# Kernel optimization log

Measured on AMD Instinct MI355X. Metric: run time of the kernel, lower is better.

Reference implementation:

```python
import jax, jax.numpy as jnp
import numpy as np

B, S, D = 16, 1024, 1024

def _xavier_uniform(key, shape, fan_in, fan_out):
    a = float(np.sqrt(6.0 / (fan_in + fan_out)))
    return jax.random.uniform(key, shape, jnp.float32, -a, a)

def setup_inputs() -> dict:
    key = jax.random.key(0)
    ks = jax.random.split(key, 8)
    query = jax.random.normal(ks[0], (B, S, D), jnp.float32)
    key_t = jax.random.normal(ks[1], (B, S, D), jnp.float32)
    value = jax.random.normal(ks[2], (B, S, D), jnp.float32)
    # learned additive attention bias [1, S, S], xavier_uniform init
    attn_bias = _xavier_uniform(ks[3], (1, S, S), S, S)
    # Linear weights (torch nn.Linear default: kaiming-uniform-ish; any init ok for baseline)
    Wq = _xavier_uniform(ks[4], (D, D), D, D)
    bq = jnp.zeros((D,), jnp.float32)
    Wk = _xavier_uniform(ks[5], (D, D), D, D)
    bk = jnp.zeros((D,), jnp.float32)
    return {"query": query, "key": key_t, "value": value,
            "attn_bias": attn_bias, "Wq": Wq, "bq": bq, "Wk": Wk, "bk": bk}

def reference(query, key, value, attn_bias, Wq, bq, Wk, bk):
    # q = query @ Wq^T + bq  (torch Linear convention)
    q = jnp.einsum('bsd,ed->bse', query, Wq) + bq            # [B,S,D]
    k = jnp.einsum('bsd,ed->bse', key, Wk) + bk              # [B,S,D]
    energy = jnp.einsum('bsd,btd->bst', q, k) + attn_bias    # [B,S,S] (bias broadcasts over B)
    attention = jax.nn.softmax(energy, axis=-1)
    out = jnp.einsum('bst,btd->bsd', attention, value)       # value is NOT projected (matches source)
    return (out, attention)
```

## Files before the change

kernel.cpp:

```cpp
#include <hip/hip_runtime.h>


#define AS1 __attribute__((address_space(1)))
#define AS3 __attribute__((address_space(3)))
#define VMCNT(n) asm volatile("s_waitcnt vmcnt(" #n ")" ::: "memory")

typedef __bf16 bf16;
typedef __bf16 bf16x4 __attribute__((ext_vector_type(4)));
typedef __bf16 bf16x8 __attribute__((ext_vector_type(8)));
typedef float  f32x4  __attribute__((ext_vector_type(4)));

constexpr int BATCH = 16;
constexpr int S = 1024;
constexpr int D = 1024;
constexpr long NBSD = (long)BATCH * S * D;

constexpr int GBM = 256, GBN = 256, GBK = 32;
constexpr int NTK = 1024 / GBK;
constexpr int ARR = GBM * GBK;

__device__ __forceinline__ void stage16(const bf16* src, const bf16* dst) {
  __builtin_amdgcn_global_load_lds((const AS1 void*)src, (AS3 void*)dst, 16, 0, 0);
}

__global__ __launch_bounds__(256) void split_convert(
    const float* __restrict__ in, bf16* __restrict__ hi, bf16* __restrict__ lo, int n4) {
  int i = blockIdx.x * blockDim.x + threadIdx.x;
  int stride = gridDim.x * blockDim.x;
  for (; i < n4; i += stride) {
    f32x4 x = ((const f32x4*)in)[i];
    bf16x4 h, l;
#pragma unroll
    for (int j = 0; j < 4; ++j) {
      float v = x[j];
      bf16 hh = (bf16)v;
      h[j] = hh;
      l[j] = (bf16)(v - (float)hh);
    }
    ((bf16x4*)hi)[i] = h;
    ((bf16x4*)lo)[i] = l;
  }
}

__global__ __launch_bounds__(256) void transpose_convert(
    const float* __restrict__ v, bf16* __restrict__ vT) {
  __shared__ float tile[32][33];
  const int b = blockIdx.z;
  const int t0 = blockIdx.y * 32, d0 = blockIdx.x * 32;
  const int tx = threadIdx.x & 31, ty = threadIdx.x >> 5;
  const float* src = v + (long)b * S * D;
#pragma unroll
  for (int i = 0; i < 4; ++i)
    tile[ty + i * 8][tx] = src[(long)(t0 + ty + i * 8) * D + d0 + tx];
  __syncthreads();
  bf16* dst = vT + (long)b * D * S;
#pragma unroll
  for (int i = 0; i < 4; ++i)
    dst[(long)(d0 + ty + i * 8) * S + t0 + tx] = (bf16)tile[tx][ty + i * 8];
}

template <int EPI>
__global__ __launch_bounds__(512, 2) void gemm8_split(
    const bf16* __restrict__ Ah_g, const bf16* __restrict__ Al_g, long a_bs,
    const bf16* __restrict__ Bh_g, const bf16* __restrict__ Bl_g, long b_bs,
    const float* __restrict__ bias,
    bf16* __restrict__ Ch, bf16* __restrict__ Cl,
    float* __restrict__ Cf, long c_bs) {
  __shared__ bf16 lds[2 * 4 * ARR];

  const int tid = threadIdx.x;
  const int lane = tid & 63, wid = tid >> 6;
  const int wr = wid >> 2, wc = wid & 3;
  const int fr = lane & 15, fq = lane >> 4;
  const int fsw = (fr >> 1) & 3;

  const int w = blockIdx.x;
  const int swz = (w & 7) * 32 + (w >> 3);
  int z, by, bx;
  if constexpr (EPI == 0) { z = 0; by = swz >> 2; bx = swz & 3; }
  else { z = swz >> 4; by = (swz >> 2) & 3; bx = swz & 3; }
  const long brow = (long)by * GBM, bcol = (long)bx * GBN;

  const bf16* A_h = Ah_g + (long)z * a_bs;
  const bf16* A_l = Al_g + (long)z * a_bs;
  const bf16* B_h = Bh_g + (long)z * b_bs;
  const bf16* B_l = Bl_g + (long)z * b_bs;

  const int srow = tid >> 2;
  const int csw = ((tid & 3) ^ ((srow >> 1) & 3)) * 8;
  const long asrc = (brow + srow) * 1024 + csw;
  const long bsrc = (bcol + srow) * 1024 + csw;
  const int dstoff = wid * 512;

  const int aoffb = (wr * 128 + fr) * 32 + (fq ^ fsw) * 8;
  const int boffb = (wc * 64 + fr) * 32 + (fq ^ fsw) * 8;

  f32x4 acc[8][4] = {};

#define STG(slot, arr, base, koff, rr) \
  stage16((base) + (koff) + (long)(rr) * 131072, \
          lds + ((slot) * 4 + (arr)) * ARR + (rr) * 4096 + dstoff)

  STG(0, 0, A_h + asrc, 0, 0); STG(0, 0, A_h + asrc, 0, 1);
  STG(0, 2, B_h + bsrc, 0, 0); STG(0, 2, B_h + bsrc, 0, 1);
  STG(0, 3, B_l + bsrc, 0, 0); STG(0, 3, B_l + bsrc, 0, 1);
  STG(0, 1, A_l + asrc, 0, 0); STG(0, 1, A_l + asrc, 0, 1);
  VMCNT(4);
  __builtin_amdgcn_s_barrier();

  for (int t = 0; t < NTK; ++t) {
    const int cur = t & 1, nxt = cur ^ 1;
    const long kn = (long)(t + 1) * GBK;
    const bf16* lA_h = lds + (cur * 4 + 0) * ARR;
    const bf16* lA_l = lds + (cur * 4 + 1) * ARR;
    const bf16* lB_h = lds + (cur * 4 + 2) * ARR;
    const bf16* lB_l = lds + (cur * 4 + 3) * ARR;

    bf16x8 ah[8], bh[4];
#pragma unroll
    for (int m = 0; m < 8; ++m) ah[m] = *(const bf16x8*)&lA_h[aoffb + m * 512];
#pragma unroll
    for (int n = 0; n < 4; ++n) bh[n] = *(const bf16x8*)&lB_h[boffb + n * 512];
    if (t + 1 < NTK) {
      STG(nxt, 0, A_h + asrc, kn, 0); STG(nxt, 0, A_h + asrc, kn, 1);
      STG(nxt, 2, B_h + bsrc, kn, 0); STG(nxt, 2, B_h + bsrc, kn, 1);
      VMCNT(6);
    } else { VMCNT(2); }
    __builtin_amdgcn_sched_barrier(0);
    __builtin_amdgcn_s_barrier();
    __builtin_amdgcn_s_setprio(1);
#pragma unroll
    for (int n = 0; n < 4; ++n)
#pragma unroll
      for (int m = 0; m < 8; ++m)
        acc[m][n] = __builtin_amdgcn_mfma_f32_16x16x32_bf16(ah[m], bh[n], acc[m][n], 0, 0, 0);
    __builtin_amdgcn_s_setprio(0);
    __builtin_amdgcn_sched_barrier(0);
    __builtin_amdgcn_s_barrier();

    bf16x8 bl[4];
#pragma unroll
    for (int n = 0; n < 4; ++n) bl[n] = *(const bf16x8*)&lB_l[boffb + n * 512];
    if (t + 1 < NTK) {
      STG(nxt, 3, B_l + bsrc, kn, 0); STG(nxt, 3, B_l + bsrc, kn, 1);
      VMCNT(6);
    } else { VMCNT(0); }
    __builtin_amdgcn_sched_barrier(0);
    __builtin_amdgcn_s_barrier();
    __builtin_amdgcn_s_setprio(1);
#pragma unroll
    for (int n = 0; n < 4; ++n)
#pragma unroll
      for (int m = 0; m < 8; ++m)
        acc[m][n] = __builtin_amdgcn_mfma_f32_16x16x32_bf16(ah[m], bl[n], acc[m][n], 0, 0, 0);
    __builtin_amdgcn_s_setprio(0);
    __builtin_amdgcn_sched_barrier(0);
    __builtin_amdgcn_s_barrier();

    bf16x8 al[8];
#pragma unroll
    for (int m = 0; m < 8; ++m) al[m] = *(const bf16x8*)&lA_l[aoffb + m * 512];
    if (t + 1 < NTK) {
      STG(nxt, 1, A_l + asrc, kn, 0); STG(nxt, 1, A_l + asrc, kn, 1);
      VMCNT(4);
    }
    __builtin_amdgcn_sched_barrier(0);
    __builtin_amdgcn_s_barrier();
    __builtin_amdgcn_s_setprio(1);
#pragma unroll
    for (int n = 0; n < 4; ++n)
#pragma unroll
      for (int m = 0; m < 8; ++m)
        acc[m][n] = __builtin_amdgcn_mfma_f32_16x16x32_bf16(al[m], bh[n], acc[m][n], 0, 0, 0);
    __builtin_amdgcn_s_setprio(0);
    __builtin_amdgcn_sched_barrier(0);
    __builtin_amdgcn_s_barrier();
  }
#undef STG

  if constexpr (EPI == 0) {
#pragma unroll
    for (int n = 0; n < 4; ++n) {
      const long col = bcol + wc * 64 + n * 16 + fr;
      const float bv = bias[col];
#pragma unroll
      for (int m = 0; m < 8; ++m) {
        const long row0 = brow + wr * 128 + m * 16 + fq * 4;
#pragma unroll
        for (int j = 0; j < 4; ++j) {
          const float c = acc[m][n][j] + bv;
          const bf16 h = (bf16)c;
          const bf16 l = (bf16)(c - (float)h);
          const long idx = (row0 + j) * 1024 + col;
          Ch[idx] = h;
          Cl[idx] = l;
        }
      }
    }
  } else {
    float* Cz = Cf + (long)z * c_bs;
#pragma unroll
    for (int n = 0; n < 4; ++n) {
      const long col = bcol + wc * 64 + n * 16 + fr;
#pragma unroll
      for (int m = 0; m < 8; ++m) {
        const long row0 = brow + wr * 128 + m * 16 + fq * 4;
#pragma unroll
        for (int j = 0; j < 4; ++j) {
          const long row = row0 + j;
          Cz[row * 1024 + col] = acc[m][n][j] + bias[row * 1024 + col];
        }
      }
    }
  }
}

__global__ __launch_bounds__(512, 2) void gemm8_plain(
    const bf16* __restrict__ A_g, long a_bs,
    const bf16* __restrict__ B_g, long b_bs,
    float* __restrict__ C, long c_bs) {
  __shared__ bf16 lds[3 * 2 * ARR];

  const int tid = threadIdx.x;
  const int lane = tid & 63, wid = tid >> 6;
  const int wr = wid >> 2, wc = wid & 3;
  const int fr = lane & 15, fq = lane >> 4;
  const int fsw = (fr >> 1) & 3;

  const int w = blockIdx.x;
  const int swz = (w & 7) * 32 + (w >> 3);
  const int z = swz >> 4, by = (swz >> 2) & 3, bx = swz & 3;
  const long brow = (long)by * GBM, bcol = (long)bx * GBN;

  const bf16* A = A_g + (long)z * a_bs;
  const bf16* B = B_g + (long)z * b_bs;

  const int srow = tid >> 2;
  const int csw = ((tid & 3) ^ ((srow >> 1) & 3)) * 8;
  const long asrc = (brow + srow) * 1024 + csw;
  const long bsrc = (bcol + srow) * 1024 + csw;
  const int dstoff = wid * 512;

  const int aoffb = (wr * 128 + fr) * 32 + (fq ^ fsw) * 8;
  const int boffb = (wc * 64 + fr) * 32 + (fq ^ fsw) * 8;

  f32x4 acc[8][4] = {};

#define STG2(slot, arr, base, koff, rr) \
  stage16((base) + (koff) + (long)(rr) * 131072, \
          lds + ((slot) * 2 + (arr)) * ARR + (rr) * 4096 + dstoff)

  STG2(0, 0, A + asrc, 0, 0);  STG2(0, 0, A + asrc, 0, 1);
  STG2(0, 1, B + bsrc, 0, 0);  STG2(0, 1, B + bsrc, 0, 1);
  STG2(1, 0, A + asrc, 32, 0); STG2(1, 0, A + asrc, 32, 1);
  STG2(1, 1, B + bsrc, 32, 0); STG2(1, 1, B + bsrc, 32, 1);
  VMCNT(4);
  __builtin_amdgcn_s_barrier();

  int cur = 0, st = 2;
  for (int t = 0; t < NTK; ++t) {
    const bf16* lA = lds + (cur * 2 + 0) * ARR;
    const bf16* lB = lds + (cur * 2 + 1) * ARR;
    bf16x8 ah[8], bh[4];
#pragma unroll
    for (int m = 0; m < 8; ++m) ah[m] = *(const bf16x8*)&lA[aoffb + m * 512];
#pragma unroll
    for (int n = 0; n < 4; ++n) bh[n] = *(const bf16x8*)&lB[boffb + n * 512];
    if (t + 2 < NTK) {
      const long kn = (long)(t + 2) * GBK;
      STG2(st, 0, A + asrc, kn, 0); STG2(st, 0, A + asrc, kn, 1);
      STG2(st, 1, B + bsrc, kn, 0); STG2(st, 1, B + bsrc, kn, 1);
      VMCNT(4);
    } else { VMCNT(0); }
    __builtin_amdgcn_sched_barrier(0);
    __builtin_amdgcn_s_barrier();
    __builtin_amdgcn_s_setprio(1);
#pragma unroll
    for (int n = 0; n < 4; ++n)
#pragma unroll
      for (int m = 0; m < 8; ++m)
        acc[m][n] = __builtin_amdgcn_mfma_f32_16x16x32_bf16(ah[m], bh[n], acc[m][n], 0, 0, 0);
    __builtin_amdgcn_s_setprio(0);
    __builtin_amdgcn_sched_barrier(0);
    __builtin_amdgcn_s_barrier();
    cur = (cur == 2) ? 0 : cur + 1;
    st  = (st == 2)  ? 0 : st + 1;
  }
#undef STG2

  float* Cz = C + (long)z * c_bs;
#pragma unroll
  for (int n = 0; n < 4; ++n) {
    const long col = bcol + wc * 64 + n * 16 + fr;
#pragma unroll
    for (int m = 0; m < 8; ++m) {
      const long row0 = brow + wr * 128 + m * 16 + fq * 4;
#pragma unroll
      for (int j = 0; j < 4; ++j)
        Cz[(row0 + j) * 1024 + col] = acc[m][n][j];
    }
  }
}

__global__ __launch_bounds__(256) void softmax_rows(
    float* __restrict__ attn, bf16* __restrict__ attn_bf) {
  const long row = blockIdx.x;
  float* p = attn + row * 1024;
  const int tid = threadIdx.x, lane = tid & 63, wid = tid >> 6;

  f32x4 x = ((const f32x4*)p)[tid];
  float m = fmaxf(fmaxf(x[0], x[1]), fmaxf(x[2], x[3]));
#pragma unroll
  for (int off = 32; off; off >>= 1) m = fmaxf(m, __shfl_xor(m, off));
  __shared__ float redm[4];
  if (lane == 0) redm[wid] = m;
  __syncthreads();
  m = fmaxf(fmaxf(redm[0], redm[1]), fmaxf(redm[2], redm[3]));

  f32x4 e;
#pragma unroll
  for (int j = 0; j < 4; ++j) e[j] = __expf(x[j] - m);
  float s = e[0] + e[1] + e[2] + e[3];
#pragma unroll
  for (int off = 32; off; off >>= 1) s += __shfl_xor(s, off);
  __shared__ float reds[4];
  if (lane == 0) reds[wid] = s;
  __syncthreads();
  s = reds[0] + reds[1] + reds[2] + reds[3];

  const float inv = 1.0f / s;
  f32x4 r;
  bf16x4 rb;
#pragma unroll
  for (int j = 0; j < 4; ++j) {
    r[j] = e[j] * inv;
    rb[j] = (bf16)r[j];
  }
  ((f32x4*)p)[tid] = r;
  ((bf16x4*)(attn_bf + row * 1024))[tid] = rb;
}

extern "C" void kernel_launch(void* const* d_in, const int* in_sizes, int n_in,
                              void* d_out, int out_size, void* d_ws, size_t ws_size,
                              hipStream_t stream) {
  const float* query     = (const float*)d_in[0];
  const float* key       = (const float*)d_in[1];
  const float* value     = (const float*)d_in[2];
  const float* attn_bias = (const float*)d_in[3];
  const float* Wq        = (const float*)d_in[4];
  const float* bq        = (const float*)d_in[5];
  const float* Wk        = (const float*)d_in[6];
  const float* bk        = (const float*)d_in[7];

  float* out  = (float*)d_out;
  float* attn = out + NBSD;

  bf16* ws    = (bf16*)d_ws;
  bf16* q_hi  = ws;
  bf16* q_lo  = ws + NBSD;
  bf16* k_hi  = ws + 2 * NBSD;
  bf16* k_lo  = ws + 3 * NBSD;
  bf16* Wq_hi = ws + 4 * NBSD;
  bf16* Wq_lo = Wq_hi + (long)D * D;
  bf16* Wk_hi = Wq_lo + (long)D * D;
  bf16* Wk_lo = Wk_hi + (long)D * D;
  bf16* scr   = Wk_lo + (long)D * D;
  bf16* key_hi = scr;
  bf16* key_lo = scr + NBSD;
  bf16* valueT  = scr;
  bf16* attn_bf = scr + NBSD;
  bf16* query_hi = (bf16*)d_out;
  bf16* query_lo = query_hi + NBSD;

  split_convert<<<2048, 256, 0, stream>>>(query, query_hi, query_lo, (int)(NBSD / 4));
  split_convert<<<2048, 256, 0, stream>>>(key, key_hi, key_lo, (int)(NBSD / 4));
  split_convert<<<512, 256, 0, stream>>>(Wq, Wq_hi, Wq_lo, D * D / 4);
  split_convert<<<512, 256, 0, stream>>>(Wk, Wk_hi, Wk_lo, D * D / 4);

  gemm8_split<0><<<256, 512, 0, stream>>>(query_hi, query_lo, 0, Wq_hi, Wq_lo, 0,
                                          bq, q_hi, q_lo, nullptr, 0);
  gemm8_split<0><<<256, 512, 0, stream>>>(key_hi, key_lo, 0, Wk_hi, Wk_lo, 0,
                                          bk, k_hi, k_lo, nullptr, 0);

  transpose_convert<<<dim3(32, 32, 16), 256, 0, stream>>>(value, valueT);

  gemm8_split<1><<<256, 512, 0, stream>>>(q_hi, q_lo, (long)S * D, k_hi, k_lo, (long)S * D,
                                          attn_bias, nullptr, nullptr, attn, (long)S * S);

  softmax_rows<<<BATCH * S, 256, 0, stream>>>(attn, attn_bf);

  gemm8_plain<<<256, 512, 0, stream>>>(attn_bf, (long)S * S, valueT, (long)D * S,
                                       out, (long)S * D);
}
```

Before: 468.3 us.

## Simplify GEMM pipelines to double-buffered with two barriers per K-step

```diff
diff --git a/kernel.cpp b/kernel.cpp
--- a/kernel.cpp
+++ b/kernel.cpp
@@ -4,6 +4,7 @@
 #define AS1 __attribute__((address_space(1)))
 #define AS3 __attribute__((address_space(3)))
 #define VMCNT(n) asm volatile("s_waitcnt vmcnt(" #n ")" ::: "memory")
+#define SBARRIER asm volatile("s_barrier" ::: "memory")
 
 typedef __bf16 bf16;
 typedef __bf16 bf16x4 __attribute__((ext_vector_type(4)));
@@ -105,76 +106,57 @@
   STG(0, 2, B_h + bsrc, 0, 0); STG(0, 2, B_h + bsrc, 0, 1);
   STG(0, 3, B_l + bsrc, 0, 0); STG(0, 3, B_l + bsrc, 0, 1);
   STG(0, 1, A_l + asrc, 0, 0); STG(0, 1, A_l + asrc, 0, 1);
-  VMCNT(4);
-  __builtin_amdgcn_s_barrier();
 
   for (int t = 0; t < NTK; ++t) {
     const int cur = t & 1, nxt = cur ^ 1;
-    const long kn = (long)(t + 1) * GBK;
     const bf16* lA_h = lds + (cur * 4 + 0) * ARR;
     const bf16* lA_l = lds + (cur * 4 + 1) * ARR;
     const bf16* lB_h = lds + (cur * 4 + 2) * ARR;
     const bf16* lB_l = lds + (cur * 4 + 3) * ARR;
 
-    bf16x8 ah[8], bh[4];
-#pragma unroll
-    for (int m = 0; m < 8; ++m) ah[m] = *(const bf16x8*)&lA_h[aoffb + m * 512];
-#pragma unroll
-    for (int n = 0; n < 4; ++n) bh[n] = *(const bf16x8*)&lB_h[boffb + n * 512];
     if (t + 1 < NTK) {
+      const long kn = (long)(t + 1) * GBK;
       STG(nxt, 0, A_h + asrc, kn, 0); STG(nxt, 0, A_h + asrc, kn, 1);
       STG(nxt, 2, B_h + bsrc, kn, 0); STG(nxt, 2, B_h + bsrc, kn, 1);
-      VMCNT(6);
-    } else { VMCNT(2); }
+      STG(nxt, 3, B_l + bsrc, kn, 0); STG(nxt, 3, B_l + bsrc, kn, 1);
+      STG(nxt, 1, A_l + asrc, kn, 0); STG(nxt, 1, A_l + asrc, kn, 1);
+      VMCNT(8);
+    } else {
+      VMCNT(0);
+    }
     __builtin_amdgcn_sched_barrier(0);
-    __builtin_amdgcn_s_barrier();
-    __builtin_amdgcn_s_setprio(1);
+    SBARRIER;
+
+    bf16x8 ah[8], bh[4];
+#pragma unroll
+    for (int m = 0; m < 8; ++m) ah[m] = *(const bf16x8*)&lA_h[aoffb + m * 512];
+#pragma unroll
+    for (int n = 0; n < 4; ++n) bh[n] = *(const bf16x8*)&lB_h[boffb + n * 512];
 #pragma unroll
     for (int n = 0; n < 4; ++n)
 #pragma unroll
       for (int m = 0; m < 8; ++m)
         acc[m][n] = __builtin_amdgcn_mfma_f32_16x16x32_bf16(ah[m], bh[n], acc[m][n], 0, 0, 0);
-    __builtin_amdgcn_s_setprio(0);
-    __builtin_amdgcn_sched_barrier(0);
-    __builtin_amdgcn_s_barrier();
 
     bf16x8 bl[4];
 #pragma unroll
     for (int n = 0; n < 4; ++n) bl[n] = *(const bf16x8*)&lB_l[boffb + n * 512];
-    if (t + 1 < NTK) {
-      STG(nxt, 3, B_l + bsrc, kn, 0); STG(nxt, 3, B_l + bsrc, kn, 1);
-      VMCNT(6);
-    } else { VMCNT(0); }
-    __builtin_amdgcn_sched_barrier(0);
-    __builtin_amdgcn_s_barrier();
-    __builtin_amdgcn_s_setprio(1);
 #pragma unroll
     for (int n = 0; n < 4; ++n)
 #pragma unroll
       for (int m = 0; m < 8; ++m)
         acc[m][n] = __builtin_amdgcn_mfma_f32_16x16x32_bf16(ah[m], bl[n], acc[m][n], 0, 0, 0);
-    __builtin_amdgcn_s_setprio(0);
-    __builtin_amdgcn_sched_barrier(0);
-    __builtin_amdgcn_s_barrier();
 
     bf16x8 al[8];
 #pragma unroll
     for (int m = 0; m < 8; ++m) al[m] = *(const bf16x8*)&lA_l[aoffb + m * 512];
-    if (t + 1 < NTK) {
-      STG(nxt, 1, A_l + asrc, kn, 0); STG(nxt, 1, A_l + asrc, kn, 1);
-      VMCNT(4);
-    }
-    __builtin_amdgcn_sched_barrier(0);
-    __builtin_amdgcn_s_barrier();
-    __builtin_amdgcn_s_setprio(1);
 #pragma unroll
     for (int n = 0; n < 4; ++n)
 #pragma unroll
       for (int m = 0; m < 8; ++m)
         acc[m][n] = __builtin_amdgcn_mfma_f32_16x16x32_bf16(al[m], bh[n], acc[m][n], 0, 0, 0);
-    __builtin_amdgcn_s_setprio(0);
-    __builtin_amdgcn_sched_barrier(0);
-    __builtin_amdgcn_s_barrier();
+
+    SBARRIER;
   }
 #undef STG
 
@@ -219,7 +201,7 @@
     const bf16* __restrict__ A_g, long a_bs,
     const bf16* __restrict__ B_g, long b_bs,
     float* __restrict__ C, long c_bs) {
-  __shared__ bf16 lds[3 * 2 * ARR];
+  __shared__ bf16 lds[2 * 2 * ARR];
 
   const int tid = threadIdx.x;
   const int lane = tid & 63, wid = tid >> 6;
@@ -250,41 +232,37 @@
   stage16((base) + (koff) + (long)(rr) * 131072, \
           lds + ((slot) * 2 + (arr)) * ARR + (rr) * 4096 + dstoff)
 
-  STG2(0, 0, A + asrc, 0, 0);  STG2(0, 0, A + asrc, 0, 1);
-  STG2(0, 1, B + bsrc, 0, 0);  STG2(0, 1, B + bsrc, 0, 1);
-  STG2(1, 0, A + asrc, 32, 0); STG2(1, 0, A + asrc, 32, 1);
-  STG2(1, 1, B + bsrc, 32, 0); STG2(1, 1, B + bsrc, 32, 1);
-  VMCNT(4);
-  __builtin_amdgcn_s_barrier();
-
-  int cur = 0, st = 2;
+  STG2(0, 0, A + asrc, 0, 0); STG2(0, 0, A + asrc, 0, 1);
+  STG2(0, 1, B + bsrc, 0, 0); STG2(0, 1, B + bsrc, 0, 1);
+
   for (int t = 0; t < NTK; ++t) {
+    const int cur = t & 1, nxt = cur ^ 1;
     const bf16* lA = lds + (cur * 2 + 0) * ARR;
     const bf16* lB = lds + (cur * 2 + 1) * ARR;
+
+    if (t + 1 < NTK) {
+      const long kn = (long)(t + 1) * GBK;
+      STG2(nxt, 0, A + asrc, kn, 0); STG2(nxt, 0, A + asrc, kn, 1);
+      STG2(nxt, 1, B + bsrc, kn, 0); STG2(nxt, 1, B + bsrc, kn, 1);
+      VMCNT(4);
+    } else {
+      VMCNT(0);
+    }
+    __builtin_amdgcn_sched_barrier(0);
+    SBARRIER;
+
     bf16x8 ah[8], bh[4];
 #pragma unroll
     for (int m = 0; m < 8; ++m) ah[m] = *(const bf16x8*)&lA[aoffb + m * 512];
 #pragma unroll
     for (int n = 0; n < 4; ++n) bh[n] = *(const bf16x8*)&lB[boffb + n * 512];
-    if (t + 2 < NTK) {
-      const long kn = (long)(t + 2) * GBK;
-      STG2(st, 0, A + asrc, kn, 0); STG2(st, 0, A + asrc, kn, 1);
-      STG2(st, 1, B + bsrc, kn, 0); STG2(st, 1, B + bsrc, kn, 1);
-      VMCNT(4);
-    } else { VMCNT(0); }
-    __builtin_amdgcn_sched_barrier(0);
-    __builtin_amdgcn_s_barrier();
-    __builtin_amdgcn_s_setprio(1);
 #pragma unroll
     for (int n = 0; n < 4; ++n)
 #pragma unroll
       for (int m = 0; m < 8; ++m)
         acc[m][n] = __builtin_amdgcn_mfma_f32_16x16x32_bf16(ah[m], bh[n], acc[m][n], 0, 0, 0);
-    __builtin_amdgcn_s_setprio(0);
-    __builtin_amdgcn_sched_barrier(0);
-    __builtin_amdgcn_s_barrier();
-    cur = (cur == 2) ? 0 : cur + 1;
-    st  = (st == 2)  ? 0 : st + 1;
+
+    SBARRIER;
   }
 #undef STG2
 
```

After: 480.8 us. 1.03x slower.
